# Optimization experiments

Hardware: AMD Instinct MI355X
Metric: run time of the kernel (lower is better)

## Reference

```python
import jax, jax.numpy as jnp
import numpy as np
import math

EMBED_DIM = 1024
NUM_HEADS = 16
D_K = EMBED_DIM // NUM_HEADS
B, S = 2, 2048


def setup_inputs() -> dict:
    key = jax.random.key(0)
    ks = jax.random.split(key, 6)
    scale = 1.0 / math.sqrt(EMBED_DIM)
    x = jax.random.normal(ks[0], (B, S, EMBED_DIM), dtype=jnp.float32)
    mask = jax.random.randint(ks[1], (B, S), 0, 2) > 0  # True = masked-out key
    wq = jax.random.normal(ks[2], (EMBED_DIM, EMBED_DIM), dtype=jnp.float32) * scale
    wk = jax.random.normal(ks[3], (EMBED_DIM, EMBED_DIM), dtype=jnp.float32) * scale
    wv = jax.random.normal(ks[4], (EMBED_DIM, EMBED_DIM), dtype=jnp.float32) * scale
    wo = jax.random.normal(ks[5], (EMBED_DIM, EMBED_DIM), dtype=jnp.float32) * scale
    return {"x": x, "mask": mask, "wq": wq, "wk": wk, "wv": wv, "wo": wo}


def reference(x, mask, wq, wk, wv, wo):
    b, s, _ = x.shape
    # torch nn.Linear(bias=False): y = x @ W.T
    q = (x @ wq.T).reshape(b, s, NUM_HEADS, D_K).transpose(0, 2, 1, 3)  # [B,H,S,Dk]
    k = (x @ wk.T).reshape(b, s, NUM_HEADS, D_K).transpose(0, 2, 1, 3)
    v = (x @ wv.T).reshape(b, s, NUM_HEADS, D_K).transpose(0, 2, 1, 3)
    scores = jnp.einsum('bhqd,bhkd->bhqk', q, k) / math.sqrt(D_K)
    # mask [B,S] -> [B,1,1,S]: key-padding mask, True filled with -1e9
    scores = jnp.where(mask[:, None, None, :], jnp.float32(-1e9), scores)
    attn = jax.nn.softmax(scores, axis=-1)
    # dropout in eval mode -> identity
    out = jnp.einsum('bhqk,bhkd->bhqd', attn, v)
    out = out.transpose(0, 2, 1, 3).reshape(b, s, EMBED_DIM)
    return out @ wo.T
```

## Files before the change

### kernel.cpp

```cpp
#include <hip/hip_runtime.h>
#include <hip/hip_bf16.h>


typedef unsigned short u16;
typedef unsigned int u32;
using short8 = __attribute__((ext_vector_type(8))) short;
using f32x4  = __attribute__((ext_vector_type(4))) float;

#define WS_XB    0u
#define WS_WQKV  8388608u
#define WS_WOB   14680064u
#define WS_QB    16777216u
#define WS_KB    25165824u
#define WS_VTB   33554432u
#define WS_OB    41943040u

__device__ __forceinline__ u16 f2bf(float f) {
  u32 u = __float_as_uint(f);
  u += 0x7fffu + ((u >> 16) & 1u);
  return (u16)(u >> 16);
}

__device__ __forceinline__ ushort4 pk4(f32x4 v) {
  ushort4 r; r.x = f2bf(v[0]); r.y = f2bf(v[1]); r.z = f2bf(v[2]); r.w = f2bf(v[3]);
  return r;
}

__device__ __forceinline__ u32 pkbf2(float lo, float hi) {
  union { __hip_bfloat162 b; u32 u; } c;
  c.b = __float22bfloat162_rn(make_float2(lo, hi));
  return c.u;
}

__device__ __forceinline__ void gload16(const void* g, void* l) {
  __builtin_amdgcn_global_load_lds(
      (const __attribute__((address_space(1))) u32*)g,
      (__attribute__((address_space(3))) u32*)l, 16, 0, 0);
}

#define KSCALE 0.18033688011112042f

__global__ void convert_k(const float* __restrict__ x, const float* __restrict__ wq,
                          const float* __restrict__ wk, const float* __restrict__ wv,
                          const float* __restrict__ wo,
                          u16* __restrict__ xb, u16* __restrict__ wqkv, u16* __restrict__ wob) {
  size_t g = ((size_t)blockIdx.x * 256 + threadIdx.x) * 4;
  const float* s; u16* d;
  if (g < 4194304u)      { s = x  + g;            d = xb   + g; }
  else if (g < 5242880u) { s = wq + (g - 4194304u); d = wqkv + (g - 4194304u); }
  else if (g < 6291456u) { s = wk + (g - 5242880u); d = wqkv + 1048576u + (g - 5242880u); }
  else if (g < 7340032u) { s = wv + (g - 6291456u); d = wqkv + 2097152u + (g - 6291456u); }
  else                   { s = wo + (g - 7340032u); d = wob  + (g - 7340032u); }
  float4 v = *(const float4*)s;
  f32x4 vv = {v.x, v.y, v.z, v.w};
  *(ushort4*)d = pk4(vv);
}

__global__ void gemm_qkv(const u16* __restrict__ A, const u16* __restrict__ Bt,
                         u16* __restrict__ qb, u16* __restrict__ kb, u16* __restrict__ vtb) {
  __shared__ __align__(16) u16 As[128 * 64];
  __shared__ __align__(16) u16 Bs[128 * 64];
  const int tid  = threadIdx.x;
  const int wave = tid >> 6, lane = tid & 63;
  const int c16  = lane & 15, quad = lane >> 4;
  const int tile_m = blockIdx.x * 128;
  const int tile_n = blockIdx.y * 128;
  const int wm = (wave >> 1) * 64, wn = (wave & 1) * 64;
  const int srow = wave * 32 + (lane >> 3);
  const int sc   = lane & 7;
  const int which = blockIdx.y >> 3;
  const bool swp  = (which < 2);

  const u16* Pa = swp ? Bs : As;
  const u16* Pb = swp ? As : Bs;
  const int  ra = swp ? wn : wm;
  const int  rb = swp ? wm : wn;

  f32x4 acc[4][4] = {};

  for (int k0 = 0; k0 < 1024; k0 += 64) {
    __syncthreads();
#pragma unroll
    for (int j = 0; j < 4; ++j) {
      int row = srow + j * 8;
      int cp  = sc ^ (row & 7);
      gload16(A  + (size_t)(tile_m + row) * 1024 + k0 + cp * 8, As + row * 64 + sc * 8);
      gload16(Bt + (size_t)(tile_n + row) * 1024 + k0 + cp * 8, Bs + row * 64 + sc * 8);
    }
    __syncthreads();
#pragma unroll
    for (int kc = 0; kc < 2; ++kc) {
      const int ch = ((kc * 4 + quad) ^ (c16 & 7)) * 8;
      short8 fa[4], fb[4];
#pragma unroll
      for (int i = 0; i < 4; ++i)
        fa[i] = *(const short8*)(Pa + (ra + i * 16 + c16) * 64 + ch);
#pragma unroll
      for (int j = 0; j < 4; ++j)
        fb[j] = *(const short8*)(Pb + (rb + j * 16 + c16) * 64 + ch);
#pragma unroll
      for (int i = 0; i < 4; ++i)
#pragma unroll
        for (int j = 0; j < 4; ++j)
          acc[i][j] = __builtin_amdgcn_mfma_f32_16x16x32_bf16(fa[i], fb[j], acc[i][j], 0, 0, 0);
    }
  }

  if (which == 2) {
#pragma unroll
    for (int i = 0; i < 4; ++i) {
      int m0 = tile_m + wm + i * 16 + quad * 4;
      int bb = m0 >> 11, ss0 = m0 & 2047;
#pragma unroll
      for (int j = 0; j < 4; ++j) {
        int f = (tile_n & 1023) + wn + j * 16 + c16;
        int h = f >> 6, d = f & 63;
        *(ushort4*)(vtb + ((size_t)(bb * 16 + h) * 64 + d) * 2048 + ss0) = pk4(acc[i][j]);
      }
    }
  } else {
    u16* dstb = which ? kb : qb;
#pragma unroll
    for (int i = 0; i < 4; ++i) {
      int full = (tile_n & 1023) + wn + i * 16 + quad * 4;
      int h = full >> 6, d0 = full & 63;
#pragma unroll
      for (int j = 0; j < 4; ++j) {
        int t = tile_m + wm + j * 16 + c16;
        int bb = t >> 11, ss = t & 2047;
        f32x4 v = acc[i][j];
        if (which == 0) { v[0] *= KSCALE; v[1] *= KSCALE; v[2] *= KSCALE; v[3] *= KSCALE; }
        *(ushort4*)(dstb + ((size_t)(bb * 16 + h) * 2048 + ss) * 64 + d0) = pk4(v);
      }
    }
  }
}

__global__ __launch_bounds__(256) void attn_k(const u16* __restrict__ qb, const u16* __restrict__ kb,
                                              const u16* __restrict__ vtb, const int* __restrict__ mask,
                                              u16* __restrict__ ob) {
  __shared__ __align__(16) u16 Ks[2][64 * 64];
  __shared__ __align__(16) u16 Vs[2][64 * 64];
  __shared__ __align__(16) u16 Ps[128 * 64];
  __shared__ u32 mask2[1024];

  const int tid  = threadIdx.x;
  const int wave = tid >> 6, lane = tid & 63;
  const int c16  = lane & 15, g4 = lane >> 4;
  const int bh   = blockIdx.y;
  const int bidx = bh >> 4, h = bh & 15;
  const int q0   = blockIdx.x * 128;

  {
    int4 m0 = *(const int4*)(mask + bidx * 2048 + tid * 8);
    int4 m1 = *(const int4*)(mask + bidx * 2048 + tid * 8 + 4);
    uint4 dd;
    dd.x = (m0.x ? 0u : 0xFFFFu) | (m0.y ? 0u : 0xFFFF0000u);
    dd.y = (m0.z ? 0u : 0xFFFFu) | (m0.w ? 0u : 0xFFFF0000u);
    dd.z = (m1.x ? 0u : 0xFFFFu) | (m1.y ? 0u : 0xFFFF0000u);
    dd.w = (m1.z ? 0u : 0xFFFFu) | (m1.w ? 0u : 0xFFFF0000u);
    *(uint4*)(mask2 + tid * 4) = dd;
  }

  const u16* qg = qb + ((size_t)bh * 2048 + q0 + wave * 32) * 64;
  short8 qf[2][2];
#pragma unroll
  for (int kc = 0; kc < 2; ++kc)
#pragma unroll
    for (int nj = 0; nj < 2; ++nj)
      qf[kc][nj] = *(const short8*)(qg + (nj * 16 + c16) * 64 + kc * 32 + g4 * 8);

  const u16* kg = kb  + (size_t)bh * 2048 * 64;
  const u16* vg = vtb + (size_t)bh * 64 * 2048;
  {
#pragma unroll
    for (int j = 0; j < 2; ++j) {
      int r  = j * 32 + (tid >> 3);
      int cp = (tid & 7) ^ (r & 7);
      gload16(kg + (size_t)r * 64 + cp * 8,   &Ks[0][j * 2048 + tid * 8]);
      gload16(vg + (size_t)r * 2048 + cp * 8, &Vs[0][j * 2048 + tid * 8]);
    }
  }
  __syncthreads();

  short8 ones;
#pragma unroll
  for (int i = 0; i < 8; ++i) ones[i] = (short)0x3F80;

  f32x4 O[2][4] = {};
  f32x4 L[2] = {};

#pragma unroll 2
  for (int kt = 0; kt < 32; ++kt) {
    if (kt) __syncthreads();
    if (kt + 1 < 32) {
      const int nb = (kt + 1) & 1;
#pragma unroll
      for (int j = 0; j < 2; ++j) {
        int r  = j * 32 + (tid >> 3);
        int cp = (tid & 7) ^ (r & 7);
        gload16(kg + (size_t)((kt + 1) * 64 + r) * 64 + cp * 8, &Ks[nb][j * 2048 + tid * 8]);
        gload16(vg + (size_t)r * 2048 + (kt + 1) * 64 + cp * 8, &Vs[nb][j * 2048 + tid * 8]);
      }
    }
    const u16* ksb = Ks[kt & 1];
    const u16* vsb = Vs[kt & 1];

    f32x4 S[4][2] = {};
#pragma unroll
    for (int kc = 0; kc < 2; ++kc) {
      const int ch = ((kc * 4 + g4) ^ (c16 & 7)) * 8;
      short8 a[4];
#pragma unroll
      for (int mi = 0; mi < 4; ++mi)
        a[mi] = *(const short8*)(ksb + (mi * 16 + c16) * 64 + ch);
#pragma unroll
      for (int mi = 0; mi < 4; ++mi)
#pragma unroll
        for (int nj = 0; nj < 2; ++nj)
          S[mi][nj] = __builtin_amdgcn_mfma_f32_16x16x32_bf16(a[mi], qf[kc][nj], S[mi][nj], 0, 0, 0);
    }

    uint2 mk[4];
#pragma unroll
    for (int mi = 0; mi < 4; ++mi)
      mk[mi] = *(const uint2*)(mask2 + kt * 32 + mi * 8 + g4 * 2);

#pragma unroll
    for (int nj = 0; nj < 2; ++nj) {
      const int q = wave * 32 + nj * 16 + c16;
#pragma unroll
      for (int mi = 0; mi < 4; ++mi) {
        float p0 = __builtin_amdgcn_exp2f(S[mi][nj][0]);
        float p1 = __builtin_amdgcn_exp2f(S[mi][nj][1]);
        float p2 = __builtin_amdgcn_exp2f(S[mi][nj][2]);
        float p3 = __builtin_amdgcn_exp2f(S[mi][nj][3]);
        u32 lo = pkbf2(p0, p1) & mk[mi].x;
        u32 hi = pkbf2(p2, p3) & mk[mi].y;
        uint2 pkd; pkd.x = lo; pkd.y = hi;
        const int c = mi * 2 + (g4 >> 1);
        *(uint2*)(Ps + q * 64 + ((c ^ (c16 & 7)) * 8 + (g4 & 1) * 4)) = pkd;
      }
    }

#pragma unroll
    for (int kc = 0; kc < 2; ++kc) {
      const int ch = ((kc * 4 + g4) ^ (c16 & 7)) * 8;
      short8 a2[2], b2[4];
#pragma unroll
      for (int mi = 0; mi < 2; ++mi)
        a2[mi] = *(const short8*)(Ps + (wave * 32 + mi * 16 + c16) * 64 + ch);
#pragma unroll
      for (int nd = 0; nd < 4; ++nd)
        b2[nd] = *(const short8*)(vsb + (nd * 16 + c16) * 64 + ch);
#pragma unroll
      for (int mi = 0; mi < 2; ++mi) {
#pragma unroll
        for (int nd = 0; nd < 4; ++nd)
          O[mi][nd] = __builtin_amdgcn_mfma_f32_16x16x32_bf16(a2[mi], b2[nd], O[mi][nd], 0, 0, 0);
        L[mi] = __builtin_amdgcn_mfma_f32_16x16x32_bf16(a2[mi], ones, L[mi], 0, 0, 0);
      }
    }
  }

  u16* og = ob + ((size_t)(bidx * 2048 + q0 + wave * 32)) * 1024 + h * 64;
#pragma unroll
  for (int mi = 0; mi < 2; ++mi) {
    f32x4 linv;
#pragma unroll
    for (int r = 0; r < 4; ++r) linv[r] = 1.f / L[mi][r];
#pragma unroll
    for (int r = 0; r < 4; ++r) {
      int qrow = mi * 16 + g4 * 4 + r;
#pragma unroll
      for (int nd = 0; nd < 4; ++nd)
        og[(size_t)qrow * 1024 + nd * 16 + c16] = f2bf(O[mi][nd][r] * linv[r]);
    }
  }
}

__global__ void gemm_out(const u16* __restrict__ A, const u16* __restrict__ Bt,
                         float* __restrict__ out) {
  __shared__ __align__(16) u16 As[128 * 64];
  __shared__ __align__(16) u16 Bs[128 * 64];
  const int tid  = threadIdx.x;
  const int wave = tid >> 6, lane = tid & 63;
  const int c16  = lane & 15, quad = lane >> 4;
  const int tile_m = blockIdx.x * 128;
  const int tile_n = blockIdx.y * 128;
  const int wm = (wave >> 1) * 64, wn = (wave & 1) * 64;
  const int srow = wave * 32 + (lane >> 3);
  const int sc   = lane & 7;

  f32x4 acc[4][4] = {};

  for (int k0 = 0; k0 < 1024; k0 += 64) {
    __syncthreads();
#pragma unroll
    for (int j = 0; j < 4; ++j) {
      int row = srow + j * 8;
      int cp  = sc ^ (row & 7);
      gload16(A  + (size_t)(tile_m + row) * 1024 + k0 + cp * 8, As + row * 64 + sc * 8);
      gload16(Bt + (size_t)(tile_n + row) * 1024 + k0 + cp * 8, Bs + row * 64 + sc * 8);
    }
    __syncthreads();
#pragma unroll
    for (int kc = 0; kc < 2; ++kc) {
      const int ch = ((kc * 4 + quad) ^ (c16 & 7)) * 8;
      short8 fa[4], fb[4];
#pragma unroll
      for (int i = 0; i < 4; ++i)
        fa[i] = *(const short8*)(Bs + (wn + i * 16 + c16) * 64 + ch);
#pragma unroll
      for (int j = 0; j < 4; ++j)
        fb[j] = *(const short8*)(As + (wm + j * 16 + c16) * 64 + ch);
#pragma unroll
      for (int i = 0; i < 4; ++i)
#pragma unroll
        for (int j = 0; j < 4; ++j)
          acc[i][j] = __builtin_amdgcn_mfma_f32_16x16x32_bf16(fa[i], fb[j], acc[i][j], 0, 0, 0);
    }
  }
#pragma unroll
  for (int i = 0; i < 4; ++i) {
    int f0 = tile_n + wn + i * 16 + quad * 4;
#pragma unroll
    for (int j = 0; j < 4; ++j) {
      int t = tile_m + wm + j * 16 + c16;
      *(f32x4*)(out + (size_t)t * 1024 + f0) = acc[i][j];
    }
  }
}

extern "C" void kernel_launch(void* const* d_in, const int* in_sizes, int n_in,
                              void* d_out, int out_size, void* d_ws, size_t ws_size,
                              hipStream_t stream) {
  (void)in_sizes; (void)n_in; (void)out_size; (void)ws_size;
  const float* x    = (const float*)d_in[0];
  const int*   mask = (const int*)d_in[1];
  const float* wq   = (const float*)d_in[2];
  const float* wk   = (const float*)d_in[3];
  const float* wv   = (const float*)d_in[4];
  const float* wo   = (const float*)d_in[5];
  float* out = (float*)d_out;
  char*  ws  = (char*)d_ws;

  u16* xb   = (u16*)(ws + WS_XB);
  u16* wqkv = (u16*)(ws + WS_WQKV);
  u16* wob  = (u16*)(ws + WS_WOB);
  u16* qbuf = (u16*)(ws + WS_QB);
  u16* kbuf = (u16*)(ws + WS_KB);
  u16* vtb  = (u16*)(ws + WS_VTB);
  u16* obuf = (u16*)(ws + WS_OB);

  convert_k<<<8192, 256, 0, stream>>>(x, wq, wk, wv, wo, xb, wqkv, wob);
  gemm_qkv<<<dim3(32, 24), 256, 0, stream>>>(xb, wqkv, qbuf, kbuf, vtb);
  attn_k<<<dim3(16, 32), 256, 0, stream>>>(qbuf, kbuf, vtb, mask, obuf);
  gemm_out<<<dim3(32, 8), 256, 0, stream>>>(obuf, wob, out);
}
```

Baseline: 185.8 us.

## Double-buffer GEMM tile loads and halve attention query tile per block

Both GEMM kernels now keep two LDS buffers and issue the global-to-LDS loads for the next K tile before computing on the current one. This overlaps memory latency with MFMA work and leaves one barrier per K step instead of two. The attention kernel drops from 128 to 64 queries per block, with each wave handling 16 query rows, and the grid doubles to 1024 blocks. That raises parallelism and cuts register and LDS use per block, but every K/V tile is now loaded twice as many times across the grid.

```diff
diff --git a/kernel.cpp b/kernel.cpp
--- a/kernel.cpp
+++ b/kernel.cpp
@@ -56,10 +56,10 @@
   *(ushort4*)d = pk4(vv);
 }
 
-__global__ void gemm_qkv(const u16* __restrict__ A, const u16* __restrict__ Bt,
+__global__ __launch_bounds__(256) void gemm_qkv(const u16* __restrict__ A, const u16* __restrict__ Bt,
                          u16* __restrict__ qb, u16* __restrict__ kb, u16* __restrict__ vtb) {
-  __shared__ __align__(16) u16 As[128 * 64];
-  __shared__ __align__(16) u16 Bs[128 * 64];
+  __shared__ __align__(16) u16 As[2][128 * 64];
+  __shared__ __align__(16) u16 Bs[2][128 * 64];
   const int tid  = threadIdx.x;
   const int wave = tid >> 6, lane = tid & 63;
   const int c16  = lane & 15, quad = lane >> 4;
@@ -68,26 +68,41 @@
   const int wm = (wave >> 1) * 64, wn = (wave & 1) * 64;
   const int srow = wave * 32 + (lane >> 3);
   const int sc   = lane & 7;
+  const int scp  = sc ^ (srow & 7);
   const int which = blockIdx.y >> 3;
   const bool swp  = (which < 2);
 
-  const u16* Pa = swp ? Bs : As;
-  const u16* Pb = swp ? As : Bs;
   const int  ra = swp ? wn : wm;
   const int  rb = swp ? wm : wn;
 
   f32x4 acc[4][4] = {};
 
-  for (int k0 = 0; k0 < 1024; k0 += 64) {
-    __syncthreads();
+  {
 #pragma unroll
     for (int j = 0; j < 4; ++j) {
       int row = srow + j * 8;
       int cp  = sc ^ (row & 7);
-      gload16(A  + (size_t)(tile_m + row) * 1024 + k0 + cp * 8, As + row * 64 + sc * 8);
-      gload16(Bt + (size_t)(tile_n + row) * 1024 + k0 + cp * 8, Bs + row * 64 + sc * 8);
-    }
+      gload16(A  + (size_t)(tile_m + row) * 1024 + cp * 8, &As[0][row * 64 + sc * 8]);
+      gload16(Bt + (size_t)(tile_n + row) * 1024 + cp * 8, &Bs[0][row * 64 + sc * 8]);
+    }
+  }
+
+#pragma unroll 2
+  for (int ki = 0; ki < 16; ++ki) {
     __syncthreads();
+    if (ki + 1 < 16) {
+      const int nb = (ki + 1) & 1;
+      const int k0 = (ki + 1) * 64;
+#pragma unroll
+      for (int j = 0; j < 4; ++j) {
+        int row = srow + j * 8;
+        int cp  = sc ^ (row & 7);
+        gload16(A  + (size_t)(tile_m + row) * 1024 + k0 + cp * 8, &As[nb][row * 64 + sc * 8]);
+        gload16(Bt + (size_t)(tile_n + row) * 1024 + k0 + cp * 8, &Bs[nb][row * 64 + sc * 8]);
+      }
+    }
+    const u16* Pa = swp ? Bs[ki & 1] : As[ki & 1];
+    const u16* Pb = swp ? As[ki & 1] : Bs[ki & 1];
 #pragma unroll
     for (int kc = 0; kc < 2; ++kc) {
       const int ch = ((kc * 4 + quad) ^ (c16 & 7)) * 8;
@@ -141,7 +156,7 @@
                                               u16* __restrict__ ob) {
   __shared__ __align__(16) u16 Ks[2][64 * 64];
   __shared__ __align__(16) u16 Vs[2][64 * 64];
-  __shared__ __align__(16) u16 Ps[128 * 64];
+  __shared__ __align__(16) u16 Ps[64 * 64];
   __shared__ u32 mask2[1024];
 
   const int tid  = threadIdx.x;
@@ -149,7 +164,7 @@
   const int c16  = lane & 15, g4 = lane >> 4;
   const int bh   = blockIdx.y;
   const int bidx = bh >> 4, h = bh & 15;
-  const int q0   = blockIdx.x * 128;
+  const int q0   = blockIdx.x * 64;
 
   {
     int4 m0 = *(const int4*)(mask + bidx * 2048 + tid * 8);
@@ -162,13 +177,11 @@
     *(uint4*)(mask2 + tid * 4) = dd;
   }
 
-  const u16* qg = qb + ((size_t)bh * 2048 + q0 + wave * 32) * 64;
-  short8 qf[2][2];
+  const u16* qg = qb + ((size_t)bh * 2048 + q0 + wave * 16) * 64;
+  short8 qf[2];
 #pragma unroll
   for (int kc = 0; kc < 2; ++kc)
-#pragma unroll
-    for (int nj = 0; nj < 2; ++nj)
-      qf[kc][nj] = *(const short8*)(qg + (nj * 16 + c16) * 64 + kc * 32 + g4 * 8);
+    qf[kc] = *(const short8*)(qg + c16 * 64 + kc * 32 + g4 * 8);
 
   const u16* kg = kb  + (size_t)bh * 2048 * 64;
   const u16* vg = vtb + (size_t)bh * 64 * 2048;
@@ -181,18 +194,17 @@
       gload16(vg + (size_t)r * 2048 + cp * 8, &Vs[0][j * 2048 + tid * 8]);
     }
   }
-  __syncthreads();
 
   short8 ones;
 #pragma unroll
   for (int i = 0; i < 8; ++i) ones[i] = (short)0x3F80;
 
-  f32x4 O[2][4] = {};
-  f32x4 L[2] = {};
+  f32x4 O[4] = {};
+  f32x4 L = {};
 
 #pragma unroll 2
   for (int kt = 0; kt < 32; ++kt) {
-    if (kt) __syncthreads();
+    __syncthreads();
     if (kt + 1 < 32) {
       const int nb = (kt + 1) & 1;
 #pragma unroll
@@ -206,19 +218,15 @@
     const u16* ksb = Ks[kt & 1];
     const u16* vsb = Vs[kt & 1];
 
-    f32x4 S[4][2] = {};
+    f32x4 S[4] = {};
 #pragma unroll
     for (int kc = 0; kc < 2; ++kc) {
       const int ch = ((kc * 4 + g4) ^ (c16 & 7)) * 8;
-      short8 a[4];
-#pragma unroll
-      for (int mi = 0; mi < 4; ++mi)
-        a[mi] = *(const short8*)(ksb + (mi * 16 + c16) * 64 + ch);
-#pragma unroll
-      for (int mi = 0; mi < 4; ++mi)
-#pragma unroll
-        for (int nj = 0; nj < 2; ++nj)
-          S[mi][nj] = __builtin_amdgcn_mfma_f32_16x16x32_bf16(a[mi], qf[kc][nj], S[mi][nj], 0, 0, 0);
+#pragma unroll
+      for (int mi = 0; mi < 4; ++mi) {
+        short8 a = *(const short8*)(ksb + (mi * 16 + c16) * 64 + ch);
+        S[mi] = __builtin_amdgcn_mfma_f32_16x16x32_bf16(a, qf[kc], S[mi], 0, 0, 0);
+      }
     }
 
     uint2 mk[4];
@@ -226,63 +234,50 @@
     for (int mi = 0; mi < 4; ++mi)
       mk[mi] = *(const uint2*)(mask2 + kt * 32 + mi * 8 + g4 * 2);
 
-#pragma unroll
-    for (int nj = 0; nj < 2; ++nj) {
-      const int q = wave * 32 + nj * 16 + c16;
-#pragma unroll
-      for (int mi = 0; mi < 4; ++mi) {
-        float p0 = __builtin_amdgcn_exp2f(S[mi][nj][0]);
-        float p1 = __builtin_amdgcn_exp2f(S[mi][nj][1]);
-        float p2 = __builtin_amdgcn_exp2f(S[mi][nj][2]);
-        float p3 = __builtin_amdgcn_exp2f(S[mi][nj][3]);
-        u32 lo = pkbf2(p0, p1) & mk[mi].x;
-        u32 hi = pkbf2(p2, p3) & mk[mi].y;
-        uint2 pkd; pkd.x = lo; pkd.y = hi;
-        const int c = mi * 2 + (g4 >> 1);
-        *(uint2*)(Ps + q * 64 + ((c ^ (c16 & 7)) * 8 + (g4 & 1) * 4)) = pkd;
-      }
+    const int q = wave * 16 + c16;
+#pragma unroll
+    for (int mi = 0; mi < 4; ++mi) {
+      float p0 = __builtin_amdgcn_exp2f(S[mi][0]);
+      float p1 = __builtin_amdgcn_exp2f(S[mi][1]);
+      float p2 = __builtin_amdgcn_exp2f(S[mi][2]);
+      float p3 = __builtin_amdgcn_exp2f(S[mi][3]);
+      uint2 pkd;
+      pkd.x = pkbf2(p0, p1) & mk[mi].x;
+      pkd.y = pkbf2(p2, p3) & mk[mi].y;
+      const int c = mi * 2 + (g4 >> 1);
+      *(uint2*)(Ps + q * 64 + ((c ^ (c16 & 7)) * 8 + (g4 & 1) * 4)) = pkd;
     }
 
 #pragma unroll
     for (int kc = 0; kc < 2; ++kc) {
       const int ch = ((kc * 4 + g4) ^ (c16 & 7)) * 8;
-      short8 a2[2], b2[4];
-#pragma unroll
-      for (int mi = 0; mi < 2; ++mi)
-        a2[mi] = *(const short8*)(Ps + (wave * 32 + mi * 16 + c16) * 64 + ch);
-#pragma unroll
-      for (int nd = 0; nd < 4; ++nd)
-        b2[nd] = *(const short8*)(vsb + (nd * 16 + c16) * 64 + ch);
-#pragma unroll
-      for (int mi = 0; mi < 2; ++mi) {
-#pragma unroll
-        for (int nd = 0; nd < 4; ++nd)
-          O[mi][nd] = __builtin_amdgcn_mfma_f32_16x16x32_bf16(a2[mi], b2[nd], O[mi][nd], 0, 0, 0);
-        L[mi] = __builtin_amdgcn_mfma_f32_16x16x32_bf16(a2[mi], ones, L[mi], 0, 0, 0);
-      }
-    }
-  }
-
-  u16* og = ob + ((size_t)(bidx * 2048 + q0 + wave * 32)) * 1024 + h * 64;
-#pragma unroll
-  for (int mi = 0; mi < 2; ++mi) {
-    f32x4 linv;
-#pragma unroll
-    for (int r = 0; r < 4; ++r) linv[r] = 1.f / L[mi][r];
-#pragma unroll
-    for (int r = 0; r < 4; ++r) {
-      int qrow = mi * 16 + g4 * 4 + r;
-#pragma unroll
-      for (int nd = 0; nd < 4; ++nd)
-        og[(size_t)qrow * 1024 + nd * 16 + c16] = f2bf(O[mi][nd][r] * linv[r]);
-    }
-  }
-}
-
-__global__ void gemm_out(const u16* __restrict__ A, const u16* __restrict__ Bt,
+      short8 a2 = *(const short8*)(Ps + (wave * 16 + c16) * 64 + ch);
+#pragma unroll
+      for (int nd = 0; nd < 4; ++nd) {
+        short8 b2 = *(const short8*)(vsb + (nd * 16 + c16) * 64 + ch);
+        O[nd] = __builtin_amdgcn_mfma_f32_16x16x32_bf16(a2, b2, O[nd], 0, 0, 0);
+      }
+      L = __builtin_amdgcn_mfma_f32_16x16x32_bf16(a2, ones, L, 0, 0, 0);
+    }
+  }
+
+  u16* og = ob + ((size_t)(bidx * 2048 + q0 + wave * 16)) * 1024 + h * 64;
+  f32x4 linv;
+#pragma unroll
+  for (int r = 0; r < 4; ++r) linv[r] = 1.f / L[r];
+#pragma unroll
+  for (int r = 0; r < 4; ++r) {
+    int qrow = g4 * 4 + r;
+#pragma unroll
+    for (int nd = 0; nd < 4; ++nd)
+      og[(size_t)qrow * 1024 + nd * 16 + c16] = f2bf(O[nd][r] * linv[r]);
+  }
+}
+
+__global__ __launch_bounds__(256) void gemm_out(const u16* __restrict__ A, const u16* __restrict__ Bt,
                          float* __restrict__ out) {
-  __shared__ __align__(16) u16 As[128 * 64];
-  __shared__ __align__(16) u16 Bs[128 * 64];
+  __shared__ __align__(16) u16 As[2][128 * 64];
+  __shared__ __align__(16) u16 Bs[2][128 * 64];
   const int tid  = threadIdx.x;
   const int wave = tid >> 6, lane = tid & 63;
   const int c16  = lane & 15, quad = lane >> 4;
@@ -294,26 +289,42 @@
 
   f32x4 acc[4][4] = {};
 
-  for (int k0 = 0; k0 < 1024; k0 += 64) {
-    __syncthreads();
+  {
 #pragma unroll
     for (int j = 0; j < 4; ++j) {
       int row = srow + j * 8;
       int cp  = sc ^ (row & 7);
-      gload16(A  + (size_t)(tile_m + row) * 1024 + k0 + cp * 8, As + row * 64 + sc * 8);
-      gload16(Bt + (size_t)(tile_n + row) * 1024 + k0 + cp * 8, Bs + row * 64 + sc * 8);
-    }
+      gload16(A  + (size_t)(tile_m + row) * 1024 + cp * 8, &As[0][row * 64 + sc * 8]);
+      gload16(Bt + (size_t)(tile_n + row) * 1024 + cp * 8, &Bs[0][row * 64 + sc * 8]);
+    }
+  }
+
+#pragma unroll 2
+  for (int ki = 0; ki < 16; ++ki) {
     __syncthreads();
+    if (ki + 1 < 16) {
+      const int nb = (ki + 1) & 1;
+      const int k0 = (ki + 1) * 64;
+#pragma unroll
+      for (int j = 0; j < 4; ++j) {
+        int row = srow + j * 8;
+        int cp  = sc ^ (row & 7);
+        gload16(A  + (size_t)(tile_m + row) * 1024 + k0 + cp * 8, &As[nb][row * 64 + sc * 8]);
+        gload16(Bt + (size_t)(tile_n + row) * 1024 + k0 + cp * 8, &Bs[nb][row * 64 + sc * 8]);
+      }
+    }
+    const u16* Pa = Bs[ki & 1];
+    const u16* Pb = As[ki & 1];
 #pragma unroll
     for (int kc = 0; kc < 2; ++kc) {
       const int ch = ((kc * 4 + quad) ^ (c16 & 7)) * 8;
       short8 fa[4], fb[4];
 #pragma unroll
       for (int i = 0; i < 4; ++i)
-        fa[i] = *(const short8*)(Bs + (wn + i * 16 + c16) * 64 + ch);
+        fa[i] = *(const short8*)(Pa + (wn + i * 16 + c16) * 64 + ch);
 #pragma unroll
       for (int j = 0; j < 4; ++j)
-        fb[j] = *(const short8*)(As + (wm + j * 16 + c16) * 64 + ch);
+        fb[j] = *(const short8*)(Pb + (wm + j * 16 + c16) * 64 + ch);
 #pragma unroll
       for (int i = 0; i < 4; ++i)
 #pragma unroll
@@ -355,6 +366,6 @@
 
   convert_k<<<8192, 256, 0, stream>>>(x, wq, wk, wv, wo, xb, wqkv, wob);
   gemm_qkv<<<dim3(32, 24), 256, 0, stream>>>(xb, wqkv, qbuf, kbuf, vtb);
-  attn_k<<<dim3(16, 32), 256, 0, stream>>>(qbuf, kbuf, vtb, mask, obuf);
+  attn_k<<<dim3(32, 32), 256, 0, stream>>>(qbuf, kbuf, vtb, mask, obuf);
   gemm_out<<<dim3(32, 8), 256, 0, stream>>>(obuf, wob, out);
 }
```

Result: slower. 222.7 us (+19.9%).
